# Kernel optimization log

Measured on AMD Instinct MI355X. Metric: run time of the kernel, lower is better.

The kernel has to match this reference:

```python
import jax, jax.numpy as jnp
import numpy as np

B, N, D = 2, 8192, 2
CIN, COUT = 6, 3
WID = 64
DEPTH = 3
M1, M2 = 12, 12
G = 64            # latent grid is G x G
K = 16            # neighbors
EDGE_IN = WID + 3 * D + 1  # 71


def _gelu(x):
    return jax.nn.gelu(x, approximate=False)  # torch nn.GELU default = exact erf


def _mlp1(x, W1, b1, W2, b2):
    # MLP(depth=1): Linear -> GELU -> Linear
    return _gelu(x @ W1 + b1) @ W2 + b2


def _mlp2(x, W1, b1, W2, b2, W3, b3):
    # MLP(depth=2): Linear -> GELU -> Linear -> GELU -> Linear
    h = _gelu(x @ W1 + b1)
    h = _gelu(h @ W2 + b2)
    return h @ W3 + b3


def _local_integral(src_c, qry_c, src_f, W1, b1, W2, b2, W3, b3):
    # src_c (B,Ns,D), qry_c (B,Nq,D), src_f (B,Ns,C) -> (B,Nq,WID)
    d2 = (jnp.sum(qry_c * qry_c, -1)[:, :, None]
          + jnp.sum(src_c * src_c, -1)[:, None, :]
          - 2.0 * jnp.einsum('bmd,bnd->bmn', qry_c, src_c))
    dist = jnp.sqrt(jnp.clip(d2, 0.0))                    # (B,Nq,Ns)
    neg, idx = jax.lax.top_k(-dist, K)                    # ascending distances
    nn_dist = -neg                                        # (B,Nq,K)
    gather = jax.vmap(lambda a, i: a[i])
    nc = gather(src_c, idx)                               # (B,Nq,K,D)
    nf = gather(src_f, idx)                               # (B,Nq,K,C)
    q = jnp.broadcast_to(qry_c[:, :, None, :], nc.shape)  # (B,Nq,K,D)
    rel = q - nc
    edge = jnp.concatenate([q, nc, rel, nn_dist[..., None], nf], axis=-1)
    # sigma = lower median of farthest-neighbor distance (torch.median semantics)
    last = jnp.sort(nn_dist[..., -1].reshape(-1))
    sigma = jnp.maximum(last[(last.shape[0] - 1) // 2], 1e-6)
    w = jnp.exp(-nn_dist[..., None] / sigma)              # (B,Nq,K,1)
    v = _mlp2(edge, W1, b1, W2, b2, W3, b3)               # (B,Nq,K,WID)
    return jnp.sum(w * v, axis=2) / jnp.clip(jnp.sum(w, axis=2), 1e-6)


def _spectral2d(x, w1, w2):
    # x (B,C,H,W); w* real-packed complex weights (Ci,Co,M1,M2,2)
    Bx, _, H, W = x.shape
    xf = jnp.fft.rfft2(x)                                 # (B,C,H,W//2+1) complex
    W1c = w1[..., 0] + 1j * w1[..., 1]
    W2c = w2[..., 0] + 1j * w2[..., 1]
    out = jnp.zeros((Bx, W1c.shape[1], H, W // 2 + 1), jnp.complex64)
    out = out.at[:, :, :M1, :M2].set(jnp.einsum('bixy,ioxy->boxy', xf[:, :, :M1, :M2], W1c))
    out = out.at[:, :, -M1:, :M2].set(jnp.einsum('bixy,ioxy->boxy', xf[:, :, -M1:, :M2], W2c))
    return jnp.fft.irfft2(out, s=(H, W))


def _fno_block(x, w1, w2, pw_W, pw_b):
    y = _spectral2d(x, w1, w2) + jnp.einsum('bihw,oi->bohw', x, pw_W) + pw_b[None, :, None, None]
    mu = jnp.mean(y, axis=(-2, -1), keepdims=True)        # InstanceNorm2d, no affine
    var = jnp.var(y, axis=(-2, -1), keepdims=True)
    return _gelu((y - mu) / jnp.sqrt(var + 1e-5))


def _latent_grid():
    ax = jnp.linspace(-1.0, 1.0, G, dtype=jnp.float32)
    gx, gy = jnp.meshgrid(ax, ax, indexing='ij')
    return jnp.stack([gx, gy], axis=-1).reshape(1, G * G, D)


def setup_inputs() -> dict:
    key = jax.random.key(0)
    ks = jax.random.split(key, 32)
    u = lambda k, sh, s: jax.random.uniform(k, sh, jnp.float32, -s, s)
    inp = {
        'coords': 2.0 * jax.random.uniform(ks[0], (B, N, D), jnp.float32) - 1.0,
        'features': jax.random.normal(ks[1], (B, N, CIN), jnp.float32),
        'lift_W1': u(ks[2], (CIN, WID), CIN ** -0.5), 'lift_b1': jnp.zeros((WID,), jnp.float32),
        'lift_W2': u(ks[3], (WID, WID), WID ** -0.5), 'lift_b2': jnp.zeros((WID,), jnp.float32),
        'gin_W1': u(ks[4], (EDGE_IN, WID), EDGE_IN ** -0.5), 'gin_b1': jnp.zeros((WID,), jnp.float32),
        'gin_W2': u(ks[5], (WID, WID), WID ** -0.5), 'gin_b2': jnp.zeros((WID,), jnp.float32),
        'gin_W3': u(ks[6], (WID, WID), WID ** -0.5), 'gin_b3': jnp.zeros((WID,), jnp.float32),
        'spec1': (1.0 / (WID * WID)) * jax.random.uniform(ks[7], (DEPTH, WID, WID, M1, M2, 2), jnp.float32),
        'spec2': (1.0 / (WID * WID)) * jax.random.uniform(ks[8], (DEPTH, WID, WID, M1, M2, 2), jnp.float32),
        'pw_W': u(ks[9], (DEPTH, WID, WID), WID ** -0.5),
        'pw_b': jnp.zeros((DEPTH, WID), jnp.float32),
        'gout_W1': u(ks[10], (EDGE_IN, WID), EDGE_IN ** -0.5), 'gout_b1': jnp.zeros((WID,), jnp.float32),
        'gout_W2': u(ks[11], (WID, WID), WID ** -0.5), 'gout_b2': jnp.zeros((WID,), jnp.float32),
        'gout_W3': u(ks[12], (WID, WID), WID ** -0.5), 'gout_b3': jnp.zeros((WID,), jnp.float32),
        'proj_W1': u(ks[13], (WID, WID), WID ** -0.5), 'proj_b1': jnp.zeros((WID,), jnp.float32),
        'proj_W2': u(ks[14], (WID, COUT), WID ** -0.5), 'proj_b2': jnp.zeros((COUT,), jnp.float32),
    }
    return inp


def reference(coords, features, lift_W1, lift_b1, lift_W2, lift_b2,
              gin_W1, gin_b1, gin_W2, gin_b2, gin_W3, gin_b3,
              spec1, spec2, pw_W, pw_b,
              gout_W1, gout_b1, gout_W2, gout_b2, gout_W3, gout_b3,
              proj_W1, proj_b1, proj_W2, proj_b2):
    grid = jnp.broadcast_to(_latent_grid(), (coords.shape[0], G * G, D))
    # lift node features
    feat = _mlp1(features, lift_W1, lift_b1, lift_W2, lift_b2)          # (B,N,WID)
    # GNO: points -> latent grid
    g = _local_integral(coords, grid, feat, gin_W1, gin_b1, gin_W2, gin_b2, gin_W3, gin_b3)
    x = g.reshape(-1, G, G, WID).transpose(0, 3, 1, 2)                  # (B,WID,G,G)
    for d in range(DEPTH):
        x = _fno_block(x, spec1[d], spec2[d], pw_W[d], pw_b[d])
    g = x.transpose(0, 2, 3, 1).reshape(-1, G * G, WID)                 # (B,G*G,WID)
    # GNO: latent grid -> points
    y = _local_integral(grid, coords, g, gout_W1, gout_b1, gout_W2, gout_b2, gout_W3, gout_b3)
    return _mlp1(y, proj_W1, proj_b1, proj_W2, proj_b2)                 # (B,N,COUT)
```

## Files before the change

### kernel.cpp

```cpp
#include <hip/hip_runtime.h>
#include <math.h>

#define B_ 2
#define N_ 8192
#define G_ 64
#define NG 4096
#define WID_ 64
#define K_ 16
#define CIN_ 6
#define COUT_ 3
#define PI_ 3.14159265358979323846

typedef unsigned long long u64k;
typedef __attribute__((ext_vector_type(8))) short bf16x8;
typedef __attribute__((ext_vector_type(16))) float f32x16;

__device__ __forceinline__ float gelu_f(float x) {
    float u = fabsf(x) * 0.70710678118654752440f;
    float t = __builtin_amdgcn_rcpf(fmaf(0.3275911f, u, 1.0f));
    float p = fmaf(fmaf(fmaf(fmaf(1.061405429f, t, -1.453152027f), t, 1.421413741f),
                        t, -0.284496736f), t, 0.254829592f) * t;
    float e = __expf(-u * u);
    float erfc_u = p * e;
    float phi = (x >= 0.f) ? fmaf(-0.5f, erfc_u, 1.0f) : (0.5f * erfc_u);
    return x * phi;
}
__device__ __forceinline__ int cellof(float v) {
    int c = (int)floorf((v + 1.0f) * 32.0f);
    return min(63, max(0, c));
}
__device__ __forceinline__ u64k umin64(u64k a, u64k b) { return a < b ? a : b; }
__device__ __forceinline__ u64k umax64(u64k a, u64k b) { return a < b ? b : a; }
__device__ __forceinline__ u64k shflxor64(u64k v, int m) {
    return (u64k)__shfl_xor((long long)v, m, 64);
}
__device__ __forceinline__ void bsort64(u64k& key, int lane) {
#pragma unroll
    for (int sz = 2; sz <= 64; sz <<= 1) {
#pragma unroll
        for (int j = sz >> 1; j >= 1; j >>= 1) {
            u64k o = shflxor64(key, j);
            bool keep_min = ((lane & j) == 0) == ((lane & sz) == 0);
            key = keep_min ? umin64(key, o) : umax64(key, o);
        }
    }
}
__device__ __forceinline__ void bmerge_into(u64k& R, u64k key, int lane) {
    u64k o = shflxor64(key, 63);
    u64k L = umin64(R, o);
#pragma unroll
    for (int j = 32; j >= 1; j >>= 1) {
        u64k t = shflxor64(L, j);
        L = ((lane & j) == 0) ? umin64(L, t) : umax64(L, t);
    }
    R = L;
}
__device__ __forceinline__ void cvt8v(float4 a, float4 b, bf16x8& hv, bf16x8& lv) {
    float v[8] = {a.x, a.y, a.z, a.w, b.x, b.y, b.z, b.w};
#pragma unroll
    for (int i = 0; i < 8; i++) {
        unsigned u = __float_as_uint(v[i]);
        unsigned r = (u + 0x8000u) & 0xffff0000u;
        hv[i] = (short)(r >> 16);
        float lo = v[i] - __uint_as_float(r);
        lv[i] = (short)(__float_as_uint(lo) >> 16);
    }
}
__device__ __forceinline__ bf16x8 ldfrag(const short* __restrict__ WB, int f, int lane) {
    return *(const bf16x8*)(WB + ((long)f * 64 + lane) * 8);
}
struct Frag4 { bf16x8 h0, l0, h1, l1; };
__device__ __forceinline__ Frag4 ldfrag4(const short* __restrict__ WB, int base, int nk,
                                         int kc, int lane) {
    Frag4 f;
    f.h0 = ldfrag(WB, base + (0 * nk + kc) * 2 + 0, lane);
    f.l0 = ldfrag(WB, base + (0 * nk + kc) * 2 + 1, lane);
    f.h1 = ldfrag(WB, base + (1 * nk + kc) * 2 + 0, lane);
    f.l1 = ldfrag(WB, base + (1 * nk + kc) * 2 + 1, lane);
    return f;
}

__global__ void k_bincount(const float2* __restrict__ coords, int* __restrict__ cnt,
                           float4* __restrict__ gp) {
    int t = blockIdx.x * blockDim.x + threadIdx.x;
    if (t < NG) {
        int i = t >> 6, j = t & 63;
        double st = 2.0 / 63.0;
        float gx = (i == 63) ? 1.0f : (float)(-1.0 + st * (double)i);
        float gy = (j == 63) ? 1.0f : (float)(-1.0 + st * (double)j);
        float s2 = __fadd_rn(__fmul_rn(gx, gx), __fmul_rn(gy, gy));
        gp[t] = make_float4(gx, gy, s2, 0.f);
    }
    if (t >= B_ * N_) return;
    float2 c = coords[t];
    int b = t >> 13;
    int cell = cellof(c.x) * 64 + cellof(c.y);
    atomicAdd(&cnt[b * 4096 + cell], 1);
}
__global__ void k_binscan(const int* __restrict__ cnt, int* __restrict__ offs) {
    int b = blockIdx.x, t = threadIdx.x;
    __shared__ int part[16];
    int4 v = ((const int4*)(cnt + b * 4096))[t];
    int sum = v.x + v.y + v.z + v.w;
    int lane = t & 63, wv = t >> 6;
    int ws = sum;
#pragma unroll
    for (int o = 1; o < 64; o <<= 1) {
        int u = __shfl_up(ws, o, 64);
        if (lane >= o) ws += u;
    }
    if (lane == 63) part[wv] = ws;
    __syncthreads();
    int base = 0;
#pragma unroll
    for (int k = 0; k < 16; k++) base += (k < wv) ? part[k] : 0;
    int incl = base + ws, excl = incl - sum;
    int* ob = offs + b * 4097;
    ob[4 * t] = excl; ob[4 * t + 1] = excl + v.x;
    ob[4 * t + 2] = excl + v.x + v.y; ob[4 * t + 3] = excl + v.x + v.y + v.z;
    if (t == 1023) ob[4096] = incl;
}
__global__ void k_binscatter(const float2* __restrict__ coords, const int* __restrict__ offs,
                             int* __restrict__ fill, float4* __restrict__ srt) {
    int t = blockIdx.x * blockDim.x + threadIdx.x;
    if (t >= B_ * N_) return;
    float2 c = coords[t];
    int b = t >> 13, n = t & 8191;
    int cell = cellof(c.x) * 64 + cellof(c.y);
    int pos = offs[b * 4097 + cell] + atomicAdd(&fill[b * 4096 + cell], 1);
    float s2 = __fadd_rn(__fmul_rn(c.x, c.x), __fmul_rn(c.y, c.y));
    srt[b * N_ + pos] = make_float4(c.x, c.y, s2, __int_as_float(n));
}

__global__ void __launch_bounds__(256) k_lift(
    const float* __restrict__ fin, const float* __restrict__ W1,
    const float* __restrict__ b1, const float* __restrict__ W2,
    const float* __restrict__ b2, float* __restrict__ fout) {
    __shared__ float xr[4][8];
    __shared__ __align__(16) float h[4][64];
    int ql = threadIdx.x >> 6, j = threadIdx.x & 63;
    int node = blockIdx.x * 4 + ql;
    if (j < CIN_) xr[ql][j] = fin[node * CIN_ + j];
    __syncthreads();
    float a = b1[j];
#pragma unroll
    for (int i = 0; i < CIN_; i++) a = fmaf(xr[ql][i], W1[i * 64 + j], a);
    h[ql][j] = gelu_f(a);
    __syncthreads();
    float a2 = b2[j];
    for (int k = 0; k < 64; k += 4) {
        float w0 = W2[(k + 0) * 64 + j], w1 = W2[(k + 1) * 64 + j];
        float w2 = W2[(k + 2) * 64 + j], w3 = W2[(k + 3) * 64 + j];
        const float4 hv = *(const float4*)&h[ql][k];
        a2 = fmaf(hv.x, w0, fmaf(hv.y, w1, fmaf(hv.z, w2, fmaf(hv.w, w3, a2))));
    }
    fout[node * 64 + j] = a2;
}

__global__ void __launch_bounds__(256) k_knn_in(
    const float4* __restrict__ gp, const float4* __restrict__ srt,
    const int* __restrict__ offs, int* __restrict__ oidx,
    float* __restrict__ odist, float* __restrict__ lastd) {
    int lane = threadIdx.x & 63;
    int w = (blockIdx.x * blockDim.x + threadIdx.x) >> 6;
    int b = w >> 12, p = w & 4095;
    float4 q = gp[p];
    float qx = q.x, qy = q.y, q2 = q.z;
    int cqx = cellof(qx), cqy = cellof(qy);
    const float4* S = srt + b * N_;
    const int* OF = offs + b * 4097;

    u64k R = ~0ull;
    u64k pend = ~0ull;
    int fill = 0;

    auto flush = [&]() {
        bsort64(pend, lane);
        bmerge_into(R, pend, lane);
        pend = ~0ull;
        fill = 0;
    };
    auto feed = [&](int s0, int s1) {
        int cnt = s1 - s0;
        while (cnt > 0) {
            int take = min(cnt, 64 - fill);
            int t = lane - fill;
            if (t >= 0 && t < take) {
                float4 sp = S[s0 + t];
                float dot = __fadd_rn(__fmul_rn(qx, sp.x), __fmul_rn(qy, sp.y));
                float d2 = __fsub_rn(__fadd_rn(q2, sp.z), 2.0f * dot);
                d2 = fmaxf(d2, 0.0f);
                pend = ((u64k)__float_as_uint(d2) << 32) | (unsigned)__float_as_int(sp.w);
            }
            fill += take; s0 += take; cnt -= take;
            if (fill == 64) flush();
        }
    };

    {
        int xa = max(cqx - 2, 0), xb = min(cqx + 2, 63);
        int ya = max(cqy - 2, 0), yb = min(cqy + 2, 63);
        for (int cx = xa; cx <= xb; cx++) feed(OF[cx * 64 + ya], OF[cx * 64 + yb + 1]);
    }
    int r = 2;
    while (true) {
        if (fill) flush();
        u64k T = (u64k)__shfl((long long)R, 15, 64);
        float d16 = __uint_as_float((unsigned)(T >> 32));
        float bm = (float)r * 0.03125f;
        if (d16 < bm * bm - 1e-5f) break;
        if (cqx - r <= 0 && cqx + r >= 63 && cqy - r <= 0 && cqy + r >= 63) break;
        r++;
        int ya = max(cqy - r, 0), yb = min(cqy + r, 63);
        if (cqx - r >= 0)  { int c0 = (cqx - r) * 64; feed(OF[c0 + ya], OF[c0 + yb + 1]); }
        if (cqx + r <= 63) { int c0 = (cqx + r) * 64; feed(OF[c0 + ya], OF[c0 + yb + 1]); }
        int xa2 = max(cqx - r + 1, 0), xb2 = min(cqx + r - 1, 63);
        for (int cx = xa2; cx <= xb2; cx++) {
            if (cqy - r >= 0)  { int cc = cx * 64 + cqy - r; feed(OF[cc], OF[cc + 1]); }
            if (cqy + r <= 63) { int cc = cx * 64 + cqy + r; feed(OF[cc], OF[cc + 1]); }
        }
    }
    if (lane < 16) {
        float d2 = __uint_as_float((unsigned)(R >> 32));
        float d = sqrtf(d2);
        oidx[w * 16 + lane] = (int)(unsigned)(R & 0xffffffffu);
        odist[w * 16 + lane] = d;
        if (lane == 15) lastd[w] = d;
    }
}

__global__ void __launch_bounds__(256) k_knn_out(
    const float2* __restrict__ coords, const float4* __restrict__ gp,
    int* __restrict__ oidx, float* __restrict__ odist, float* __restrict__ lastd) {
    int lane = threadIdx.x & 63;
    int w = (blockIdx.x * blockDim.x + threadIdx.x) >> 6;
    float2 c = coords[w];
    float qx = c.x, qy = c.y;
    float q2 = __fadd_rn(__fmul_rn(qx, qx), __fmul_rn(qy, qy));
    int i0 = (int)floorf((qx + 1.0f) * 31.5f);
    int j0 = (int)floorf((qy + 1.0f) * 31.5f);
    int li = min(max(i0 - 3, 0), 56);
    int lj = min(max(j0 - 3, 0), 56);
    int p = (li + (lane >> 3)) * 64 + (lj + (lane & 7));
    float4 sp = gp[p];
    float dot = __fadd_rn(__fmul_rn(qx, sp.x), __fmul_rn(qy, sp.y));
    float d2 = fmaxf(__fsub_rn(__fadd_rn(q2, sp.z), 2.0f * dot), 0.0f);
    u64k key = ((u64k)__float_as_uint(d2) << 32) | (unsigned)p;
    bsort64(key, lane);
    if (lane < 16) {
        float dd = sqrtf(__uint_as_float((unsigned)(key >> 32)));
        oidx[w * 16 + lane] = (int)(unsigned)(key & 0xffffffffu);
        odist[w * 16 + lane] = dd;
        if (lane == 15) lastd[w] = dd;
    }
}

__global__ void __launch_bounds__(1024) k_median_bis(
    const float* __restrict__ vals, int n, float* __restrict__ sig) {
    __shared__ int wred[2][16];
    int tid = threadIdx.x;
    int lane = tid & 63, wv = tid >> 6;
    int cnt_per = n >> 10;
    unsigned v[16];
    for (int i = 0; i < cnt_per; i++) v[i] = __float_as_uint(vals[tid + (i << 10)]);
    int r = (n - 1) >> 1;
    unsigned prefix = 0;
    for (int bit = 31; bit >= 0; bit--) {
        unsigned cand = prefix | (1u << bit);
        int c = 0;
        for (int i = 0; i < cnt_per; i++) c += (v[i] < cand) ? 1 : 0;
        for (int o = 32; o >= 1; o >>= 1) c += __shfl_down(c, o, 64);
        int buf = bit & 1;
        if (lane == 0) wred[buf][wv] = c;
        __syncthreads();
        int tot = 0;
#pragma unroll
        for (int k = 0; k < 16; k++) tot += wred[buf][k];
        prefix = (tot <= r) ? cand : prefix;
    }
    if (tid == 0) *sig = fmaxf(__uint_as_float(prefix), 1e-6f);
}

__global__ void k_wcvt(const float* __restrict__ W1a, const float* __restrict__ W2a,
                       const float* __restrict__ W3a, short* __restrict__ WBa,
                       const float* __restrict__ W1b, const float* __restrict__ W2b,
                       const float* __restrict__ W3b, short* __restrict__ WBb) {
    int t = blockIdx.x * blockDim.x + threadIdx.x;
    if (t >= 6656) return;
    int setb = (t >= 3328);
    int tt = t - (setb ? 3328 : 0);
    const float* W1s = setb ? W1b : W1a;
    const float* W2s = setb ? W2b : W2a;
    const float* W3s = setb ? W3b : W3a;
    short* WB = setb ? WBb : WBa;
    int f = tt >> 6, lane = tt & 63;
    const float* W; int h, nt, kc, l1 = 0;
    if (f < 20)      { W = W1s; int r = f;      h = r & 1; r >>= 1; nt = r / 5; kc = r % 5; l1 = 1; }
    else if (f < 36) { W = W2s; int r = f - 20; h = r & 1; r >>= 1; nt = r / 4; kc = r % 4; }
    else             { W = W3s; int r = f - 36; h = r & 1; r >>= 1; nt = r / 4; kc = r % 4; }
    int col = nt * 32 + (lane & 31);
    bf16x8 out;
#pragma unroll
    for (int i = 0; i < 8; i++) {
        int k = kc * 16 + (lane >> 5) * 8 + i;
        float w = 0.f;
        if (l1) {
            if (k < 7) w = W[k * 64 + col];
            else if (k >= 8 && k < 72) w = W[(k - 1) * 64 + col];
        } else {
            w = W[k * 64 + col];
        }
        unsigned u = __float_as_uint(w);
        unsigned hi = (u + 0x7fffu + ((u >> 16) & 1u)) & 0xffff0000u;
        float lo = w - __uint_as_float(hi);
        unsigned ul = __float_as_uint(lo);
        unsigned lr = ul + 0x7fffu + ((ul >> 16) & 1u);
        out[i] = h ? (short)(lr >> 16) : (short)(hi >> 16);
    }
    *(bf16x8*)(WB + ((long)f * 64 + lane) * 8) = out;
}

template <int MODE>
__global__ void __launch_bounds__(128, 4) k_edge_mfma(
    const int* __restrict__ idxb, const float* __restrict__ distb,
    const float* __restrict__ sigp,
    const float2* __restrict__ coords, const float4* __restrict__ gp,
    const float* __restrict__ feats, const short* __restrict__ WB,
    const float* __restrict__ b1, const float* __restrict__ b2,
    const float* __restrict__ b3,
    float* __restrict__ outb) {
    constexpr int QSH  = (MODE == 0) ? 12 : 13;
    constexpr int QMSK = (MODE == 0) ? 4095 : 8191;
    constexpr long SR  = (MODE == 0) ? 8192 : 4096;
    __shared__ float X[2][2432];
    const int tid = threadIdx.x, wv = tid >> 6, lane = tid & 63;
    const int r31 = lane & 31, g = lane >> 5;
    const int qbase = (blockIdx.x * 2 + wv) * 2;
    const float sig = *sigp;
    float* X_ = X[wv];

    Frag4 cur = ldfrag4(WB, 0, 5, 0, lane);

    int si = 0; float wt = 0.f;
    if (lane < 32) {
        int q = lane >> 4, e = lane & 15;
        int gq = qbase + q;
        int b = gq >> QSH, p = gq & QMSK;
        si = idxb[gq * 16 + e];
        float d = distb[gq * 16 + e];
        wt = __expf(-d / sig);
        float qx, qy, sx, sy;
        if (MODE == 0) {
            float4 gv = gp[p]; qx = gv.x; qy = gv.y;
            float2 cc = coords[(long)b * SR + si]; sx = cc.x; sy = cc.y;
        } else {
            float2 cc = coords[gq]; qx = cc.x; qy = cc.y;
            float4 gv = gp[si]; sx = gv.x; sy = gv.y;
        }
        float* row = X_ + lane * 76;
        *(float4*)row       = make_float4(qx, qy, sx, sy);
        *(float4*)(row + 4) = make_float4(qx - sx, qy - sy, d, 0.f);
    }
    float swt = wt;
#pragma unroll
    for (int m = 1; m < 16; m <<= 1) swt += __shfl_xor(swt, m, 64);
    {
        float4 fv[8];
#pragma unroll
        for (int it = 0; it < 8; it++) {
            int slot = it * 64 + lane;
            int row = slot >> 4, f4 = slot & 15;
            int gq = qbase + (row >> 4);
            int b = gq >> QSH;
            int sr = __shfl(si, row, 64);
            fv[it] = *(const float4*)&feats[((long)b * SR + sr) * 64 + f4 * 4];
        }
#pragma unroll
        for (int it = 0; it < 8; it++) {
            int slot = it * 64 + lane;
            int row = slot >> 4, f4 = slot & 15;
            *(float4*)&X_[row * 76 + 8 + f4 * 4] = fv[it];
        }
    }

    f32x16 acc0, acc1;
    float4 xa, xb;
    {
        float bb0 = b1[r31], bb1 = b1[32 + r31];
#pragma unroll
        for (int i = 0; i < 16; i++) { acc0[i] = bb0; acc1[i] = bb1; }
        {
            const float* xp = &X_[r31 * 76 + g * 8];
            xa = *(const float4*)xp; xb = *(const float4*)(xp + 4);
        }
#pragma unroll
        for (int kc = 0; kc < 5; kc++) {
            Frag4 nxt = (kc < 4) ? ldfrag4(WB, 0, 5, kc + 1, lane)
                                 : ldfrag4(WB, 20, 4, 0, lane);
            bf16x8 ah, al;
            if (kc == 4 && g) {
#pragma unroll
                for (int i = 0; i < 8; i++) { ah[i] = 0; al[i] = 0; }
            } else {
                cvt8v(xa, xb, ah, al);
            }
            if (kc < 4 && (kc != 3 || g == 0)) {
                const float* xp = &X_[r31 * 76 + (kc + 1) * 16 + g * 8];
                xa = *(const float4*)xp; xb = *(const float4*)(xp + 4);
            }
            __builtin_amdgcn_s_setprio(1);
            acc0 = __builtin_amdgcn_mfma_f32_32x32x16_bf16(ah, cur.h0, acc0, 0, 0, 0);
            acc1 = __builtin_amdgcn_mfma_f32_32x32x16_bf16(ah, cur.h1, acc1, 0, 0, 0);
            acc0 = __builtin_amdgcn_mfma_f32_32x32x16_bf16(al, cur.h0, acc0, 0, 0, 0);
            acc1 = __builtin_amdgcn_mfma_f32_32x32x16_bf16(al, cur.h1, acc1, 0, 0, 0);
            acc0 = __builtin_amdgcn_mfma_f32_32x32x16_bf16(ah, cur.l0, acc0, 0, 0, 0);
            acc1 = __builtin_amdgcn_mfma_f32_32x32x16_bf16(ah, cur.l1, acc1, 0, 0, 0);
            __builtin_amdgcn_s_setprio(0);
            cur = nxt;
        }
    }
#pragma unroll
    for (int reg = 0; reg < 16; reg++) {
        int row = (reg & 3) + 8 * (reg >> 2) + 4 * g;
        X_[row * 76 + r31]      = gelu_f(acc0[reg]);
        X_[row * 76 + 32 + r31] = gelu_f(acc1[reg]);
    }
    {
        float bb0 = b2[r31], bb1 = b2[32 + r31];
#pragma unroll
        for (int i = 0; i < 16; i++) { acc0[i] = bb0; acc1[i] = bb1; }
        {
            const float* xp = &X_[r31 * 76 + g * 8];
            xa = *(const float4*)xp; xb = *(const float4*)(xp + 4);
        }
#pragma unroll
        for (int kc = 0; kc < 4; kc++) {
            Frag4 nxt = (kc < 3) ? ldfrag4(WB, 20, 4, kc + 1, lane)
                                 : ldfrag4(WB, 36, 4, 0, lane);
            bf16x8 ah, al;
            cvt8v(xa, xb, ah, al);
            if (kc < 3) {
                const float* xp = &X_[r31 * 76 + (kc + 1) * 16 + g * 8];
                xa = *(const float4*)xp; xb = *(const float4*)(xp + 4);
            }
            __builtin_amdgcn_s_setprio(1);
            acc0 = __builtin_amdgcn_mfma_f32_32x32x16_bf16(ah, cur.h0, acc0, 0, 0, 0);
            acc1 = __builtin_amdgcn_mfma_f32_32x32x16_bf16(ah, cur.h1, acc1, 0, 0, 0);
            acc0 = __builtin_amdgcn_mfma_f32_32x32x16_bf16(al, cur.h0, acc0, 0, 0, 0);
            acc1 = __builtin_amdgcn_mfma_f32_32x32x16_bf16(al, cur.h1, acc1, 0, 0, 0);
            acc0 = __builtin_amdgcn_mfma_f32_32x32x16_bf16(ah, cur.l0, acc0, 0, 0, 0);
            acc1 = __builtin_amdgcn_mfma_f32_32x32x16_bf16(ah, cur.l1, acc1, 0, 0, 0);
            __builtin_amdgcn_s_setprio(0);
            cur = nxt;
        }
    }
#pragma unroll
    for (int reg = 0; reg < 16; reg++) {
        int row = (reg & 3) + 8 * (reg >> 2) + 4 * g;
        X_[row * 76 + r31]      = gelu_f(acc0[reg]);
        X_[row * 76 + 32 + r31] = gelu_f(acc1[reg]);
    }
    {
        float bb0 = b3[r31], bb1 = b3[32 + r31];
#pragma unroll
        for (int i = 0; i < 16; i++) { acc0[i] = bb0; acc1[i] = bb1; }
        {
            const float* xp = &X_[r31 * 76 + g * 8];
            xa = *(const float4*)xp; xb = *(const float4*)(xp + 4);
        }
#pragma unroll
        for (int kc = 0; kc < 4; kc++) {
            Frag4 nxt = cur;
            if (kc < 3) nxt = ldfrag4(WB, 36, 4, kc + 1, lane);
            bf16x8 ah, al;
            cvt8v(xa, xb, ah, al);
            if (kc < 3) {
                const float* xp = &X_[r31 * 76 + (kc + 1) * 16 + g * 8];
                xa = *(const float4*)xp; xb = *(const float4*)(xp + 4);
            }
            __builtin_amdgcn_s_setprio(1);
            acc0 = __builtin_amdgcn_mfma_f32_32x32x16_bf16(ah, cur.h0, acc0, 0, 0, 0);
            acc1 = __builtin_amdgcn_mfma_f32_32x32x16_bf16(ah, cur.h1, acc1, 0, 0, 0);
            acc0 = __builtin_amdgcn_mfma_f32_32x32x16_bf16(al, cur.h0, acc0, 0, 0, 0);
            acc1 = __builtin_amdgcn_mfma_f32_32x32x16_bf16(al, cur.h1, acc1, 0, 0, 0);
            acc0 = __builtin_amdgcn_mfma_f32_32x32x16_bf16(ah, cur.l0, acc0, 0, 0, 0);
            acc1 = __builtin_amdgcn_mfma_f32_32x32x16_bf16(ah, cur.l1, acc1, 0, 0, 0);
            __builtin_amdgcn_s_setprio(0);
            cur = nxt;
        }
    }
    float wtv[16];
#pragma unroll
    for (int reg = 0; reg < 16; reg++)
        wtv[reg] = __shfl(wt, (reg & 3) + 8 * (reg >> 2) + 4 * g, 64);
    float s00 = 0.f, s01 = 0.f, s10 = 0.f, s11 = 0.f;
#pragma unroll
    for (int reg = 0; reg < 16; reg++) {
        if (reg < 8) { s00 = fmaf(wtv[reg], acc0[reg], s00); s01 = fmaf(wtv[reg], acc1[reg], s01); }
        else         { s10 = fmaf(wtv[reg], acc0[reg], s10); s11 = fmaf(wtv[reg], acc1[reg], s11); }
    }
    s00 += __shfl_xor(s00, 32, 64);
    s01 += __shfl_xor(s01, 32, 64);
    s10 += __shfl_xor(s10, 32, 64);
    s11 += __shfl_xor(s11, 32, 64);
    float sw0 = __shfl(swt, 0, 64), sw1 = __shfl(swt, 16, 64);
    if (g == 0) {
        float i0 = 1.0f / fmaxf(sw0, 1e-6f), i1 = 1.0f / fmaxf(sw1, 1e-6f);
        int gq0 = qbase, gq1 = qbase + 1;
        if (MODE == 0) {
            int b0 = gq0 >> QSH, p0 = gq0 & QMSK;
            int b1i = gq1 >> QSH, p1 = gq1 & QMSK;
            outb[((long)b0 * 64 + r31) * 4096 + p0]        = s00 * i0;
            outb[((long)b0 * 64 + 32 + r31) * 4096 + p0]   = s01 * i0;
            outb[((long)b1i * 64 + r31) * 4096 + p1]       = s10 * i1;
            outb[((long)b1i * 64 + 32 + r31) * 4096 + p1]  = s11 * i1;
        } else {
            outb[(long)gq0 * 64 + r31]      = s00 * i0;
            outb[(long)gq0 * 64 + 32 + r31] = s01 * i0;
            outb[(long)gq1 * 64 + r31]      = s10 * i1;
            outb[(long)gq1 * 64 + 32 + r31] = s11 * i1;
        }
    }
}

__global__ void k_transp(const float* __restrict__ src, float* __restrict__ dst, int R, int C) {
    __shared__ float t[32][33];
    int b = blockIdx.z;
    int c0 = blockIdx.x * 32, r0 = blockIdx.y * 32;
    int tx = threadIdx.x, ty0 = threadIdx.y;
    for (int yy = ty0; yy < 32; yy += 8) {
        int r = r0 + yy, c = c0 + tx;
        if (r < R && c < C) t[yy][tx] = src[((long)b * R + r) * C + c];
    }
    __syncthreads();
    for (int yy = ty0; yy < 32; yy += 8) {
        int c = c0 + yy, r = r0 + tx;
        if (r < R && c < C) dst[((long)b * C + c) * R + r] = t[tx][yy];
    }
}

__global__ void __launch_bounds__(384) k_f1(const float* __restrict__ x, float* __restrict__ Xh) {
    int blk = blockIdx.x >> 1;
    int chalf = blockIdx.x & 1;
    int tid = threadIdx.x;
    __shared__ __align__(16) float img[4096];
    __shared__ float Tre[64][6], Tim[64][6];
    __shared__ float cs[64], sn[64];
    if (tid < 64) {
        double a = (2.0 * PI_ / 64.0) * (double)tid;
        cs[tid] = (float)cos(a);
        sn[tid] = (float)sin(a);
    }
    for (int t = tid; t < 1024; t += 384)
        ((float4*)img)[t] = ((const float4*)(x + (long)blk * 4096))[t];
    __syncthreads();
    {
        int h = tid / 6, cl = tid - 6 * h;
        int c = chalf * 6 + cl;
        float cr = cs[c], sr = sn[c];
        float pr = 1.f, pi = 0.f;
        float re = 0.f, im = 0.f;
#pragma unroll 16
        for (int w = 0; w < 64; w++) {
            if (w == 32) {
                int k = (c * 32) & 63;
                pr = cs[k]; pi = sn[k];
            }
            float v = img[h * 64 + w];
            re = fmaf(v, pr, re);
            im = fmaf(-v, pi, im);
            float nr = pr * cr - pi * sr;
            pi = fmaf(pr, sr, pi * cr);
            pr = nr;
        }
        Tre[h][cl] = re; Tim[h][cl] = im;
    }
    __syncthreads();
    if (tid < 144) {
        int xx = tid / 6, cl = tid - 6 * xx;
        int r = (xx < 12) ? xx : (xx + 40);
        float cr = cs[r], sr = sn[r];
        float pr = 1.f, pi = 0.f;
        float re = 0.f, im = 0.f;
#pragma unroll 16
        for (int h = 0; h < 64; h++) {
            if (h == 32) {
                int k = (r * 32) & 63;
                pr = cs[k]; pi = sn[k];
            }
            float a = Tre[h][cl], bb = Tim[h][cl];
            re += a * pr + bb * pi;
            im += bb * pr - a * pi;
            float nr = pr * cr - pi * sr;
            pi = fmaf(pr, sr, pi * cr);
            pr = nr;
        }
        int m = xx * 12 + chalf * 6 + cl;
        Xh[((long)blk * 288 + m) * 2] = re;
        Xh[((long)blk * 288 + m) * 2 + 1] = im;
    }
}

__global__ void __launch_bounds__(320) k_f2(const float* __restrict__ Xh, const float* __restrict__ s1,
                                            const float* __restrict__ s2, float* __restrict__ Yh) {
    int bo = blockIdx.x;
    int b = bo >> 6, o = bo & 63;
    int m = threadIdx.x;
    if (m >= 288) return;
    int xx = m / 12, y = m - 12 * xx;
    const float* W; int xw;
    if (xx < 12) { W = s1; xw = xx; } else { W = s2; xw = xx - 12; }
    long wbase = (long)o * 288 + xw * 24 + y * 2;
    const float* Xb = Xh + ((long)b * 64) * 576;
    float re = 0.f, im = 0.f;
    for (int i = 0; i < 64; i++) {
        float2 wv = *(const float2*)&W[(long)i * 18432 + wbase];
        float2 xv = *(const float2*)&Xb[(long)i * 576 + m * 2];
        re += xv.x * wv.x - xv.y * wv.y;
        im += xv.x * wv.y + xv.y * wv.x;
    }
    float* Yb = Yh + (((long)b * 64 + o) * 288 + m) * 2;
    Yb[0] = re; Yb[1] = im;
}

__global__ void __launch_bounds__(1024) k_f3(const float* __restrict__ Yh, const float* __restrict__ x,
                                             const float* __restrict__ pwW, const float* __restrict__ pwb,
                                             float* __restrict__ xo) {
    int blk = blockIdx.x;
    int b = blk >> 6, o = blk & 63;
    int tid = threadIdx.x;
    __shared__ float yre[288], yim[288];
    __shared__ float Qre[64][12], Qim[64][12];
    __shared__ float cs[64], sn[64];
    __shared__ float red[16];
    if (tid < 64) {
        double a = (2.0 * PI_ / 64.0) * (double)tid;
        cs[tid] = (float)cos(a);
        sn[tid] = (float)sin(a);
    }
    if (tid < 288) {
        yre[tid] = Yh[((long)blk * 288 + tid) * 2];
        yim[tid] = Yh[((long)blk * 288 + tid) * 2 + 1];
    }
    __syncthreads();
    if (tid < 768) {
        int h = tid / 12, c = tid - 12 * h;
        float re = 0.f, im = 0.f;
#pragma unroll
        for (int xx = 0; xx < 24; xx++) {
            int r = (xx < 12) ? xx : (xx + 40);
            int k = (r * h) & 63;
            float wr = cs[k], wi = sn[k];
            float a = yre[xx * 12 + c], bb = yim[xx * 12 + c];
            re += a * wr - bb * wi;
            im += a * wi + bb * wr;
        }
        Qre[h][c] = re * (1.0f / 64.0f);
        Qim[h][c] = im * (1.0f / 64.0f);
    }
    __syncthreads();
    float bias = pwb[o];
    int h = tid >> 4;
    int w0 = (tid & 15) * 4;
    float sp0, sp1, sp2, sp3;
    {
        float base = Qre[h][0];
        sp0 = sp1 = sp2 = sp3 = base;
#pragma unroll
        for (int c = 1; c < 12; c++) {
            float qr = Qre[h][c], qi = Qim[h][c];
            int k0 = (c * w0) & 63, k1 = (c * (w0 + 1)) & 63;
            int k2 = (c * (w0 + 2)) & 63, k3 = (c * (w0 + 3)) & 63;
            sp0 += 2.0f * (qr * cs[k0] - qi * sn[k0]);
            sp1 += 2.0f * (qr * cs[k1] - qi * sn[k1]);
            sp2 += 2.0f * (qr * cs[k2] - qi * sn[k2]);
            sp3 += 2.0f * (qr * cs[k3] - qi * sn[k3]);
        }
    }
    float a0 = sp0 * (1.0f / 64.0f) + bias;
    float a1 = sp1 * (1.0f / 64.0f) + bias;
    float a2 = sp2 * (1.0f / 64.0f) + bias;
    float a3 = sp3 * (1.0f / 64.0f) + bias;
    const float* xb = x + ((long)b * 64) * 4096 + tid * 4;
    for (int i = 0; i < 64; i++) {
        float wv = pwW[o * 64 + i];
        const float4 xv = *(const float4*)(xb + (long)i * 4096);
        a0 = fmaf(xv.x, wv, a0);
        a1 = fmaf(xv.y, wv, a1);
        a2 = fmaf(xv.z, wv, a2);
        a3 = fmaf(xv.w, wv, a3);
    }
    float ssum = a0 + a1 + a2 + a3;
#pragma unroll
    for (int m = 1; m < 64; m <<= 1) ssum += __shfl_xor(ssum, m, 64);
    if ((tid & 63) == 0) red[tid >> 6] = ssum;
    __syncthreads();
    float mu = 0.f;
#pragma unroll
    for (int k = 0; k < 16; k++) mu += red[k];
    mu *= (1.0f / 4096.0f);
    __syncthreads();
    float d0 = a0 - mu, d1 = a1 - mu, d2 = a2 - mu, d3 = a3 - mu;
    float sq = d0 * d0 + d1 * d1 + d2 * d2 + d3 * d3;
#pragma unroll
    for (int m = 1; m < 64; m <<= 1) sq += __shfl_xor(sq, m, 64);
    if ((tid & 63) == 0) red[tid >> 6] = sq;
    __syncthreads();
    float var = 0.f;
#pragma unroll
    for (int k = 0; k < 16; k++) var += red[k];
    var *= (1.0f / 4096.0f);
    float inv = 1.0f / sqrtf(var + 1e-5f);
    float4 ov = make_float4(gelu_f(d0 * inv), gelu_f(d1 * inv), gelu_f(d2 * inv), gelu_f(d3 * inv));
    *(float4*)&xo[(long)blk * 4096 + tid * 4] = ov;
}

__global__ void __launch_bounds__(256) k_proj(
    const float* __restrict__ y, const float* __restrict__ W1, const float* __restrict__ b1,
    const float* __restrict__ W2, const float* __restrict__ b2, float* __restrict__ out) {
    __shared__ __align__(16) float yr[4][64];
    __shared__ float h[4][64];
    int ql = threadIdx.x >> 6, j = threadIdx.x & 63;
    long node = (long)blockIdx.x * 4 + ql;
    yr[ql][j] = y[node * 64 + j];
    __syncthreads();
    float a = b1[j];
    for (int k = 0; k < 64; k += 4) {
        float w0 = W1[(k + 0) * 64 + j], w1 = W1[(k + 1) * 64 + j];
        float w2 = W1[(k + 2) * 64 + j], w3 = W1[(k + 3) * 64 + j];
        const float4 hv = *(const float4*)&yr[ql][k];
        a = fmaf(hv.x, w0, fmaf(hv.y, w1, fmaf(hv.z, w2, fmaf(hv.w, w3, a))));
    }
    h[ql][j] = gelu_f(a);
    __syncthreads();
    if (j < 3) {
        float a2 = b2[j];
        for (int k = 0; k < 64; k++) a2 = fmaf(h[ql][k], W2[k * 3 + j], a2);
        out[node * 3 + j] = a2;
    }
}

extern "C" void kernel_launch(void* const* d_in, const int* in_sizes, int n_in,
                              void* d_out, int out_size, void* d_ws, size_t ws_size,
                              hipStream_t stream) {
    (void)in_sizes; (void)n_in; (void)out_size; (void)ws_size;
    const float* coords   = (const float*)d_in[0];
    const float* features = (const float*)d_in[1];
    const float* lift_W1 = (const float*)d_in[2];
    const float* lift_b1 = (const float*)d_in[3];
    const float* lift_W2 = (const float*)d_in[4];
    const float* lift_b2 = (const float*)d_in[5];
    const float* gin_W1 = (const float*)d_in[6];
    const float* gin_b1 = (const float*)d_in[7];
    const float* gin_W2 = (const float*)d_in[8];
    const float* gin_b2 = (const float*)d_in[9];
    const float* gin_W3 = (const float*)d_in[10];
    const float* gin_b3 = (const float*)d_in[11];
    const float* spec1 = (const float*)d_in[12];
    const float* spec2 = (const float*)d_in[13];
    const float* pw_W  = (const float*)d_in[14];
    const float* pw_b  = (const float*)d_in[15];
    const float* gout_W1 = (const float*)d_in[16];
    const float* gout_b1 = (const float*)d_in[17];
    const float* gout_W2 = (const float*)d_in[18];
    const float* gout_b2 = (const float*)d_in[19];
    const float* gout_W3 = (const float*)d_in[20];
    const float* gout_b3 = (const float*)d_in[21];
    const float* proj_W1 = (const float*)d_in[22];
    const float* proj_b1 = (const float*)d_in[23];
    const float* proj_W2 = (const float*)d_in[24];
    const float* proj_b2 = (const float*)d_in[25];

    char* ws = (char*)d_ws;
    size_t off = 0;
    auto alloc = [&](size_t bytes) -> char* {
        char* p = ws + off;
        off = (off + bytes + 255) & ~(size_t)255;
        return p;
    };
    float4* grid_pack = (float4*)alloc((size_t)NG * 16);
    float*  feat      = (float*)alloc((size_t)B_ * N_ * 64 * 4);
    int*    bin_cnt   = (int*)alloc((size_t)B_ * 4096 * 4);
    int*    bin_fill  = (int*)alloc((size_t)B_ * 4096 * 4);
    int*    bin_off   = (int*)alloc((size_t)B_ * 4097 * 4);
    float4* srt       = (float4*)alloc((size_t)B_ * N_ * 16);
    int*    idx_in    = (int*)alloc((size_t)B_ * NG * 16 * 4);
    float*  dist_in   = (float*)alloc((size_t)B_ * NG * 16 * 4);
    float*  lastd_in  = (float*)alloc((size_t)B_ * NG * 4);
    float*  sig_in    = (float*)alloc(256);
    float*  xb0       = (float*)alloc((size_t)B_ * 64 * NG * 4);
    float*  xb1       = (float*)alloc((size_t)B_ * 64 * NG * 4);
    float*  Xh        = (float*)alloc((size_t)B_ * 64 * 288 * 2 * 4);
    float*  Yh        = (float*)alloc((size_t)B_ * 64 * 288 * 2 * 4);
    float*  g2        = (float*)alloc((size_t)B_ * NG * 64 * 4);
    int*    idx_out   = (int*)alloc((size_t)B_ * N_ * 16 * 4);
    float*  dist_out  = (float*)alloc((size_t)B_ * N_ * 16 * 4);
    float*  lastd_out = (float*)alloc((size_t)B_ * N_ * 4);
    float*  sig_out   = (float*)alloc(256);
    float*  ybuf      = (float*)alloc((size_t)B_ * N_ * 64 * 4);
    short*  wb_in     = (short*)alloc((size_t)52 * 1024);
    short*  wb_out    = (short*)alloc((size_t)52 * 1024);

    hipMemsetAsync(bin_cnt, 0, (size_t)B_ * 4096 * 4 * 2, stream);

    k_wcvt<<<26, 256, 0, stream>>>(gin_W1, gin_W2, gin_W3, wb_in,
                                   gout_W1, gout_W2, gout_W3, wb_out);
    k_lift<<<(B_ * N_) / 4, 256, 0, stream>>>(features, lift_W1, lift_b1, lift_W2, lift_b2, feat);
    k_bincount<<<(B_ * N_) / 256, 256, 0, stream>>>((const float2*)coords, bin_cnt, grid_pack);
    k_binscan<<<B_, 1024, 0, stream>>>(bin_cnt, bin_off);
    k_binscatter<<<(B_ * N_) / 256, 256, 0, stream>>>((const float2*)coords, bin_off, bin_fill, srt);
    k_knn_in<<<(B_ * NG * 64) / 256, 256, 0, stream>>>(grid_pack, srt, bin_off, idx_in, dist_in, lastd_in);
    k_median_bis<<<1, 1024, 0, stream>>>(lastd_in, B_ * NG, sig_in);
    k_edge_mfma<0><<<(B_ * NG) / 4, 128, 0, stream>>>(idx_in, dist_in, sig_in,
        (const float2*)coords, grid_pack, feat, wb_in,
        gin_b1, gin_b2, gin_b3, xb0);
    float* xc = xb0; float* xn = xb1;
    for (int d = 0; d < 3; d++) {
        k_f1<<<B_ * 64 * 2, 384, 0, stream>>>(xc, Xh);
        k_f2<<<B_ * 64, 320, 0, stream>>>(Xh, spec1 + (size_t)d * 1179648, spec2 + (size_t)d * 1179648, Yh);
        k_f3<<<B_ * 64, 1024, 0, stream>>>(Yh, xc, pw_W + (size_t)d * 4096, pw_b + (size_t)d * 64, xn);
        float* tmp = xc; xc = xn; xn = tmp;
    }
    {
        dim3 g(NG / 32, 64 / 32, B_); dim3 t(32, 8);
        k_transp<<<g, t, 0, stream>>>(xc, g2, 64, NG);
    }
    k_knn_out<<<(B_ * N_ * 64) / 256, 256, 0, stream>>>((const float2*)coords, grid_pack, idx_out, dist_out, lastd_out);
    k_median_bis<<<1, 1024, 0, stream>>>(lastd_out, B_ * N_, sig_out);
    k_edge_mfma<1><<<(B_ * N_) / 4, 128, 0, stream>>>(idx_out, dist_out, sig_out,
        (const float2*)coords, grid_pack, g2, wb_out,
        gout_b1, gout_b2, gout_b3, ybuf);
    k_proj<<<(B_ * N_) / 4, 256, 0, stream>>>(ybuf, proj_W1, proj_b1, proj_W2, proj_b2, (float*)d_out);
}
```

Before: 403.8 us.

## Merge prep kernels, both kNN searches, and both median passes into fewer launches

Several small independent kernels are combined into single launches by branching on block index. Lift MLP, weight conversion, grid packing and bin zeroing now run as one prep kernel, replacing a memset. The in and out kNN searches are fused into one launch, and both sigma medians into one two-block kernel, which moves the out-side kNN ahead of the FNO blocks. This removes launch overhead and lets independent work share the GPU, at the cost of larger, branchier kernels.

```diff
diff --git a/kernel.cpp b/kernel.cpp
--- a/kernel.cpp
+++ b/kernel.cpp
@@ -80,17 +80,86 @@
     return f;
 }
 
-__global__ void k_bincount(const float2* __restrict__ coords, int* __restrict__ cnt,
-                           float4* __restrict__ gp) {
-    int t = blockIdx.x * blockDim.x + threadIdx.x;
-    if (t < NG) {
+__global__ void __launch_bounds__(256) k_prep(
+    const float* __restrict__ fin, const float* __restrict__ lW1,
+    const float* __restrict__ lb1, const float* __restrict__ lW2,
+    const float* __restrict__ lb2, float* __restrict__ fout,
+    const float* __restrict__ W1a, const float* __restrict__ W2a,
+    const float* __restrict__ W3a, short* __restrict__ WBa,
+    const float* __restrict__ W1b, const float* __restrict__ W2b,
+    const float* __restrict__ W3b, short* __restrict__ WBb,
+    float4* __restrict__ gp, int* __restrict__ bins) {
+    __shared__ float xr[4][8];
+    __shared__ __align__(16) float h[4][64];
+    int blk = blockIdx.x;
+    if (blk < 4096) {
+        int ql = threadIdx.x >> 6, j = threadIdx.x & 63;
+        int node = blk * 4 + ql;
+        if (j < CIN_) xr[ql][j] = fin[node * CIN_ + j];
+        __syncthreads();
+        float a = lb1[j];
+#pragma unroll
+        for (int i = 0; i < CIN_; i++) a = fmaf(xr[ql][i], lW1[i * 64 + j], a);
+        h[ql][j] = gelu_f(a);
+        __syncthreads();
+        float a2 = lb2[j];
+        for (int k = 0; k < 64; k += 4) {
+            float w0 = lW2[(k + 0) * 64 + j], w1 = lW2[(k + 1) * 64 + j];
+            float w2 = lW2[(k + 2) * 64 + j], w3 = lW2[(k + 3) * 64 + j];
+            const float4 hv = *(const float4*)&h[ql][k];
+            a2 = fmaf(hv.x, w0, fmaf(hv.y, w1, fmaf(hv.z, w2, fmaf(hv.w, w3, a2))));
+        }
+        fout[node * 64 + j] = a2;
+    } else if (blk < 4122) {
+        int t = (blk - 4096) * 256 + threadIdx.x;
+        if (t >= 6656) return;
+        int setb = (t >= 3328);
+        int tt = t - (setb ? 3328 : 0);
+        const float* W1s = setb ? W1b : W1a;
+        const float* W2s = setb ? W2b : W2a;
+        const float* W3s = setb ? W3b : W3a;
+        short* WB = setb ? WBb : WBa;
+        int f = tt >> 6, lane = tt & 63;
+        const float* W; int hh, nt, kc, l1 = 0;
+        if (f < 20)      { W = W1s; int r = f;      hh = r & 1; r >>= 1; nt = r / 5; kc = r % 5; l1 = 1; }
+        else if (f < 36) { W = W2s; int r = f - 20; hh = r & 1; r >>= 1; nt = r / 4; kc = r % 4; }
+        else             { W = W3s; int r = f - 36; hh = r & 1; r >>= 1; nt = r / 4; kc = r % 4; }
+        int col = nt * 32 + (lane & 31);
+        bf16x8 out;
+#pragma unroll
+        for (int i = 0; i < 8; i++) {
+            int k = kc * 16 + (lane >> 5) * 8 + i;
+            float w = 0.f;
+            if (l1) {
+                if (k < 7) w = W[k * 64 + col];
+                else if (k >= 8 && k < 72) w = W[(k - 1) * 64 + col];
+            } else {
+                w = W[k * 64 + col];
+            }
+            unsigned u = __float_as_uint(w);
+            unsigned hi = (u + 0x7fffu + ((u >> 16) & 1u)) & 0xffff0000u;
+            float lo = w - __uint_as_float(hi);
+            unsigned ul = __float_as_uint(lo);
+            unsigned lr = ul + 0x7fffu + ((ul >> 16) & 1u);
+            out[i] = hh ? (short)(lr >> 16) : (short)(hi >> 16);
+        }
+        *(bf16x8*)(WB + ((long)f * 64 + lane) * 8) = out;
+    } else if (blk < 4138) {
+        int t = (blk - 4122) * 256 + threadIdx.x;
         int i = t >> 6, j = t & 63;
         double st = 2.0 / 63.0;
         float gx = (i == 63) ? 1.0f : (float)(-1.0 + st * (double)i);
         float gy = (j == 63) ? 1.0f : (float)(-1.0 + st * (double)j);
         float s2 = __fadd_rn(__fmul_rn(gx, gx), __fmul_rn(gy, gy));
         gp[t] = make_float4(gx, gy, s2, 0.f);
-    }
+    } else {
+        int t = (blk - 4138) * 256 + threadIdx.x;
+        bins[t] = 0;
+    }
+}
+
+__global__ void k_bincount(const float2* __restrict__ coords, int* __restrict__ cnt) {
+    int t = blockIdx.x * blockDim.x + threadIdx.x;
     if (t >= B_ * N_) return;
     float2 c = coords[t];
     int b = t >> 13;
@@ -132,131 +201,108 @@
     srt[b * N_ + pos] = make_float4(c.x, c.y, s2, __int_as_float(n));
 }
 
-__global__ void __launch_bounds__(256) k_lift(
-    const float* __restrict__ fin, const float* __restrict__ W1,
-    const float* __restrict__ b1, const float* __restrict__ W2,
-    const float* __restrict__ b2, float* __restrict__ fout) {
-    __shared__ float xr[4][8];
-    __shared__ __align__(16) float h[4][64];
-    int ql = threadIdx.x >> 6, j = threadIdx.x & 63;
-    int node = blockIdx.x * 4 + ql;
-    if (j < CIN_) xr[ql][j] = fin[node * CIN_ + j];
-    __syncthreads();
-    float a = b1[j];
-#pragma unroll
-    for (int i = 0; i < CIN_; i++) a = fmaf(xr[ql][i], W1[i * 64 + j], a);
-    h[ql][j] = gelu_f(a);
-    __syncthreads();
-    float a2 = b2[j];
-    for (int k = 0; k < 64; k += 4) {
-        float w0 = W2[(k + 0) * 64 + j], w1 = W2[(k + 1) * 64 + j];
-        float w2 = W2[(k + 2) * 64 + j], w3 = W2[(k + 3) * 64 + j];
-        const float4 hv = *(const float4*)&h[ql][k];
-        a2 = fmaf(hv.x, w0, fmaf(hv.y, w1, fmaf(hv.z, w2, fmaf(hv.w, w3, a2))));
-    }
-    fout[node * 64 + j] = a2;
-}
-
-__global__ void __launch_bounds__(256) k_knn_in(
+__global__ void __launch_bounds__(256) k_knn(
     const float4* __restrict__ gp, const float4* __restrict__ srt,
-    const int* __restrict__ offs, int* __restrict__ oidx,
-    float* __restrict__ odist, float* __restrict__ lastd) {
+    const int* __restrict__ offs, const float2* __restrict__ coords,
+    int* __restrict__ oidx_in, float* __restrict__ odist_in, float* __restrict__ lastd_in,
+    int* __restrict__ oidx_out, float* __restrict__ odist_out, float* __restrict__ lastd_out) {
     int lane = threadIdx.x & 63;
-    int w = (blockIdx.x * blockDim.x + threadIdx.x) >> 6;
-    int b = w >> 12, p = w & 4095;
-    float4 q = gp[p];
-    float qx = q.x, qy = q.y, q2 = q.z;
-    int cqx = cellof(qx), cqy = cellof(qy);
-    const float4* S = srt + b * N_;
-    const int* OF = offs + b * 4097;
-
-    u64k R = ~0ull;
-    u64k pend = ~0ull;
-    int fill = 0;
-
-    auto flush = [&]() {
-        bsort64(pend, lane);
-        bmerge_into(R, pend, lane);
-        pend = ~0ull;
-        fill = 0;
-    };
-    auto feed = [&](int s0, int s1) {
-        int cnt = s1 - s0;
-        while (cnt > 0) {
-            int take = min(cnt, 64 - fill);
-            int t = lane - fill;
-            if (t >= 0 && t < take) {
-                float4 sp = S[s0 + t];
-                float dot = __fadd_rn(__fmul_rn(qx, sp.x), __fmul_rn(qy, sp.y));
-                float d2 = __fsub_rn(__fadd_rn(q2, sp.z), 2.0f * dot);
-                d2 = fmaxf(d2, 0.0f);
-                pend = ((u64k)__float_as_uint(d2) << 32) | (unsigned)__float_as_int(sp.w);
+    if (blockIdx.x < 2048) {
+        int w = (blockIdx.x * blockDim.x + threadIdx.x) >> 6;
+        int b = w >> 12, p = w & 4095;
+        float4 q = gp[p];
+        float qx = q.x, qy = q.y, q2 = q.z;
+        int cqx = cellof(qx), cqy = cellof(qy);
+        const float4* S = srt + b * N_;
+        const int* OF = offs + b * 4097;
+
+        u64k R = ~0ull;
+        u64k pend = ~0ull;
+        int fill = 0;
+
+        auto flush = [&]() {
+            bsort64(pend, lane);
+            bmerge_into(R, pend, lane);
+            pend = ~0ull;
+            fill = 0;
+        };
+        auto feed = [&](int s0, int s1) {
+            int cnt = s1 - s0;
+            while (cnt > 0) {
+                int take = min(cnt, 64 - fill);
+                int t = lane - fill;
+                if (t >= 0 && t < take) {
+                    float4 sp = S[s0 + t];
+                    float dot = __fadd_rn(__fmul_rn(qx, sp.x), __fmul_rn(qy, sp.y));
+                    float d2 = __fsub_rn(__fadd_rn(q2, sp.z), 2.0f * dot);
+                    d2 = fmaxf(d2, 0.0f);
+                    pend = ((u64k)__float_as_uint(d2) << 32) | (unsigned)__float_as_int(sp.w);
+                }
+                fill += take; s0 += take; cnt -= take;
+                if (fill == 64) flush();
             }
-            fill += take; s0 += take; cnt -= take;
-            if (fill == 64) flush();
-        }
-    };
-
-    {
-        int xa = max(cqx - 2, 0), xb = min(cqx + 2, 63);
-        int ya = max(cqy - 2, 0), yb = min(cqy + 2, 63);
-        for (int cx = xa; cx <= xb; cx++) feed(OF[cx * 64 + ya], OF[cx * 64 + yb + 1]);
-    }
-    int r = 2;
-    while (true) {
-        if (fill) flush();
-        u64k T = (u64k)__shfl((long long)R, 15, 64);
-        float d16 = __uint_as_float((unsigned)(T >> 32));
-        float bm = (float)r * 0.03125f;
-        if (d16 < bm * bm - 1e-5f) break;
-        if (cqx - r <= 0 && cqx + r >= 63 && cqy - r <= 0 && cqy + r >= 63) break;
-        r++;
-        int ya = max(cqy - r, 0), yb = min(cqy + r, 63);
-        if (cqx - r >= 0)  { int c0 = (cqx - r) * 64; feed(OF[c0 + ya], OF[c0 + yb + 1]); }
-        if (cqx + r <= 63) { int c0 = (cqx + r) * 64; feed(OF[c0 + ya], OF[c0 + yb + 1]); }
-        int xa2 = max(cqx - r + 1, 0), xb2 = min(cqx + r - 1, 63);
-        for (int cx = xa2; cx <= xb2; cx++) {
-            if (cqy - r >= 0)  { int cc = cx * 64 + cqy - r; feed(OF[cc], OF[cc + 1]); }
-            if (cqy + r <= 63) { int cc = cx * 64 + cqy + r; feed(OF[cc], OF[cc + 1]); }
-        }
-    }
-    if (lane < 16) {
-        float d2 = __uint_as_float((unsigned)(R >> 32));
-        float d = sqrtf(d2);
-        oidx[w * 16 + lane] = (int)(unsigned)(R & 0xffffffffu);
-        odist[w * 16 + lane] = d;
-        if (lane == 15) lastd[w] = d;
-    }
-}
-
-__global__ void __launch_bounds__(256) k_knn_out(
-    const float2* __restrict__ coords, const float4* __restrict__ gp,
-    int* __restrict__ oidx, float* __restrict__ odist, float* __restrict__ lastd) {
-    int lane = threadIdx.x & 63;
-    int w = (blockIdx.x * blockDim.x + threadIdx.x) >> 6;
-    float2 c = coords[w];
-    float qx = c.x, qy = c.y;
-    float q2 = __fadd_rn(__fmul_rn(qx, qx), __fmul_rn(qy, qy));
-    int i0 = (int)floorf((qx + 1.0f) * 31.5f);
-    int j0 = (int)floorf((qy + 1.0f) * 31.5f);
-    int li = min(max(i0 - 3, 0), 56);
-    int lj = min(max(j0 - 3, 0), 56);
-    int p = (li + (lane >> 3)) * 64 + (lj + (lane & 7));
-    float4 sp = gp[p];
-    float dot = __fadd_rn(__fmul_rn(qx, sp.x), __fmul_rn(qy, sp.y));
-    float d2 = fmaxf(__fsub_rn(__fadd_rn(q2, sp.z), 2.0f * dot), 0.0f);
-    u64k key = ((u64k)__float_as_uint(d2) << 32) | (unsigned)p;
-    bsort64(key, lane);
-    if (lane < 16) {
-        float dd = sqrtf(__uint_as_float((unsigned)(key >> 32)));
-        oidx[w * 16 + lane] = (int)(unsigned)(key & 0xffffffffu);
-        odist[w * 16 + lane] = dd;
-        if (lane == 15) lastd[w] = dd;
-    }
-}
-
-__global__ void __launch_bounds__(1024) k_median_bis(
-    const float* __restrict__ vals, int n, float* __restrict__ sig) {
+        };
+
+        {
+            int xa = max(cqx - 2, 0), xb = min(cqx + 2, 63);
+            int ya = max(cqy - 2, 0), yb = min(cqy + 2, 63);
+            for (int cx = xa; cx <= xb; cx++) feed(OF[cx * 64 + ya], OF[cx * 64 + yb + 1]);
+        }
+        int r = 2;
+        while (true) {
+            if (fill) flush();
+            u64k T = (u64k)__shfl((long long)R, 15, 64);
+            float d16 = __uint_as_float((unsigned)(T >> 32));
+            float bm = (float)r * 0.03125f;
+            if (d16 < bm * bm - 1e-5f) break;
+            if (cqx - r <= 0 && cqx + r >= 63 && cqy - r <= 0 && cqy + r >= 63) break;
+            r++;
+            int ya = max(cqy - r, 0), yb = min(cqy + r, 63);
+            if (cqx - r >= 0)  { int c0 = (cqx - r) * 64; feed(OF[c0 + ya], OF[c0 + yb + 1]); }
+            if (cqx + r <= 63) { int c0 = (cqx + r) * 64; feed(OF[c0 + ya], OF[c0 + yb + 1]); }
+            int xa2 = max(cqx - r + 1, 0), xb2 = min(cqx + r - 1, 63);
+            for (int cx = xa2; cx <= xb2; cx++) {
+                if (cqy - r >= 0)  { int cc = cx * 64 + cqy - r; feed(OF[cc], OF[cc + 1]); }
+                if (cqy + r <= 63) { int cc = cx * 64 + cqy + r; feed(OF[cc], OF[cc + 1]); }
+            }
+        }
+        if (lane < 16) {
+            float d2 = __uint_as_float((unsigned)(R >> 32));
+            float d = sqrtf(d2);
+            oidx_in[w * 16 + lane] = (int)(unsigned)(R & 0xffffffffu);
+            odist_in[w * 16 + lane] = d;
+            if (lane == 15) lastd_in[w] = d;
+        }
+    } else {
+        int w = ((blockIdx.x - 2048) * blockDim.x + threadIdx.x) >> 6;
+        float2 c = coords[w];
+        float qx = c.x, qy = c.y;
+        float q2 = __fadd_rn(__fmul_rn(qx, qx), __fmul_rn(qy, qy));
+        int i0 = (int)floorf((qx + 1.0f) * 31.5f);
+        int j0 = (int)floorf((qy + 1.0f) * 31.5f);
+        int li = min(max(i0 - 3, 0), 56);
+        int lj = min(max(j0 - 3, 0), 56);
+        int p = (li + (lane >> 3)) * 64 + (lj + (lane & 7));
+        float4 sp = gp[p];
+        float dot = __fadd_rn(__fmul_rn(qx, sp.x), __fmul_rn(qy, sp.y));
+        float d2 = fmaxf(__fsub_rn(__fadd_rn(q2, sp.z), 2.0f * dot), 0.0f);
+        u64k key = ((u64k)__float_as_uint(d2) << 32) | (unsigned)p;
+        bsort64(key, lane);
+        if (lane < 16) {
+            float dd = sqrtf(__uint_as_float((unsigned)(key >> 32)));
+            oidx_out[w * 16 + lane] = (int)(unsigned)(key & 0xffffffffu);
+            odist_out[w * 16 + lane] = dd;
+            if (lane == 15) lastd_out[w] = dd;
+        }
+    }
+}
+
+__global__ void __launch_bounds__(1024) k_median2(
+    const float* __restrict__ vin, const float* __restrict__ vout,
+    float* __restrict__ sig_in, float* __restrict__ sig_out) {
+    const float* vals = blockIdx.x ? vout : vin;
+    int n = blockIdx.x ? (B_ * N_) : (B_ * NG);
+    float* sig = blockIdx.x ? sig_out : sig_in;
     __shared__ int wred[2][16];
     int tid = threadIdx.x;
     int lane = tid & 63, wv = tid >> 6;
@@ -279,45 +325,6 @@
         prefix = (tot <= r) ? cand : prefix;
     }
     if (tid == 0) *sig = fmaxf(__uint_as_float(prefix), 1e-6f);
-}
-
-__global__ void k_wcvt(const float* __restrict__ W1a, const float* __restrict__ W2a,
-                       const float* __restrict__ W3a, short* __restrict__ WBa,
-                       const float* __restrict__ W1b, const float* __restrict__ W2b,
-                       const float* __restrict__ W3b, short* __restrict__ WBb) {
-    int t = blockIdx.x * blockDim.x + threadIdx.x;
-    if (t >= 6656) return;
-    int setb = (t >= 3328);
-    int tt = t - (setb ? 3328 : 0);
-    const float* W1s = setb ? W1b : W1a;
-    const float* W2s = setb ? W2b : W2a;
-    const float* W3s = setb ? W3b : W3a;
-    short* WB = setb ? WBb : WBa;
-    int f = tt >> 6, lane = tt & 63;
-    const float* W; int h, nt, kc, l1 = 0;
-    if (f < 20)      { W = W1s; int r = f;      h = r & 1; r >>= 1; nt = r / 5; kc = r % 5; l1 = 1; }
-    else if (f < 36) { W = W2s; int r = f - 20; h = r & 1; r >>= 1; nt = r / 4; kc = r % 4; }
-    else             { W = W3s; int r = f - 36; h = r & 1; r >>= 1; nt = r / 4; kc = r % 4; }
-    int col = nt * 32 + (lane & 31);
-    bf16x8 out;
-#pragma unroll
-    for (int i = 0; i < 8; i++) {
-        int k = kc * 16 + (lane >> 5) * 8 + i;
-        float w = 0.f;
-        if (l1) {
-            if (k < 7) w = W[k * 64 + col];
-            else if (k >= 8 && k < 72) w = W[(k - 1) * 64 + col];
-        } else {
-            w = W[k * 64 + col];
-        }
-        unsigned u = __float_as_uint(w);
-        unsigned hi = (u + 0x7fffu + ((u >> 16) & 1u)) & 0xffff0000u;
-        float lo = w - __uint_as_float(hi);
-        unsigned ul = __float_as_uint(lo);
-        unsigned lr = ul + 0x7fffu + ((ul >> 16) & 1u);
-        out[i] = h ? (short)(lr >> 16) : (short)(hi >> 16);
-    }
-    *(bf16x8*)(WB + ((long)f * 64 + lane) * 8) = out;
 }
 
 template <int MODE>
@@ -801,16 +808,17 @@
     short*  wb_in     = (short*)alloc((size_t)52 * 1024);
     short*  wb_out    = (short*)alloc((size_t)52 * 1024);
 
-    hipMemsetAsync(bin_cnt, 0, (size_t)B_ * 4096 * 4 * 2, stream);
-
-    k_wcvt<<<26, 256, 0, stream>>>(gin_W1, gin_W2, gin_W3, wb_in,
-                                   gout_W1, gout_W2, gout_W3, wb_out);
-    k_lift<<<(B_ * N_) / 4, 256, 0, stream>>>(features, lift_W1, lift_b1, lift_W2, lift_b2, feat);
-    k_bincount<<<(B_ * N_) / 256, 256, 0, stream>>>((const float2*)coords, bin_cnt, grid_pack);
+    k_prep<<<4202, 256, 0, stream>>>(features, lift_W1, lift_b1, lift_W2, lift_b2, feat,
+                                     gin_W1, gin_W2, gin_W3, wb_in,
+                                     gout_W1, gout_W2, gout_W3, wb_out,
+                                     grid_pack, bin_cnt);
+    k_bincount<<<(B_ * N_) / 256, 256, 0, stream>>>((const float2*)coords, bin_cnt);
     k_binscan<<<B_, 1024, 0, stream>>>(bin_cnt, bin_off);
     k_binscatter<<<(B_ * N_) / 256, 256, 0, stream>>>((const float2*)coords, bin_off, bin_fill, srt);
-    k_knn_in<<<(B_ * NG * 64) / 256, 256, 0, stream>>>(grid_pack, srt, bin_off, idx_in, dist_in, lastd_in);
-    k_median_bis<<<1, 1024, 0, stream>>>(lastd_in, B_ * NG, sig_in);
+    k_knn<<<2048 + 4096, 256, 0, stream>>>(grid_pack, srt, bin_off, (const float2*)coords,
+                                           idx_in, dist_in, lastd_in,
+                                           idx_out, dist_out, lastd_out);
+    k_median2<<<2, 1024, 0, stream>>>(lastd_in, lastd_out, sig_in, sig_out);
     k_edge_mfma<0><<<(B_ * NG) / 4, 128, 0, stream>>>(idx_in, dist_in, sig_in,
         (const float2*)coords, grid_pack, feat, wb_in,
         gin_b1, gin_b2, gin_b3, xb0);
@@ -825,8 +833,6 @@
         dim3 g(NG / 32, 64 / 32, B_); dim3 t(32, 8);
         k_transp<<<g, t, 0, stream>>>(xc, g2, 64, NG);
     }
-    k_knn_out<<<(B_ * N_ * 64) / 256, 256, 0, stream>>>((const float2*)coords, grid_pack, idx_out, dist_out, lastd_out);
-    k_median_bis<<<1, 1024, 0, stream>>>(lastd_out, B_ * N_, sig_out);
     k_edge_mfma<1><<<(B_ * N_) / 4, 128, 0, stream>>>(idx_out, dist_out, sig_out,
         (const float2*)coords, grid_pack, g2, wb_out,
         gout_b1, gout_b2, gout_b3, ybuf);
```

New measurement: 363.0 us. 10.1% less time.
